# Kernel tuning notes

Hardware: AMD Instinct MI355X
Metric: run time of the kernel (lower is better)

## Reference

```python
import math
import jax, jax.numpy as jnp
import numpy as np

N_HEAD = 16
BLOCK_SIZE = 2048


def setup_inputs() -> dict:
    key = jax.random.key(0)
    ks = jax.random.split(key, 6)
    B, L, D = 2, 2048, 1024
    hs = D // N_HEAD
    s = 0.02
    return {
        "x": jax.random.normal(ks[0], (B, L, D), dtype=jnp.float32),
        "Wqkv": jax.random.normal(ks[1], (D, 3 * D), dtype=jnp.float32) * s,
        "bqkv": jax.random.normal(ks[2], (3 * D,), dtype=jnp.float32) * s,
        "Wproj": jax.random.normal(ks[3], (D, D), dtype=jnp.float32) * s,
        "bproj": jax.random.normal(ks[4], (D,), dtype=jnp.float32) * s,
        "Er": jax.random.normal(ks[5], (BLOCK_SIZE, hs), dtype=jnp.float32),
    }


def _skew(QEr):
    # QEr: [B, H, L, L] -> pad one zero column on the left, reshape, drop first row
    B, H, R, C = QEr.shape
    padded = jnp.pad(QEr, ((0, 0), (0, 0), (0, 0), (1, 0)))  # [B,H,R,C+1]
    reshaped = padded.reshape(B, H, C + 1, R)
    return reshaped[:, :, 1:, :]  # [B,H,R,C]


def reference(x, Wqkv, bqkv, Wproj, bproj, Er):
    B, L, D = x.shape
    H = N_HEAD
    hs = D // H
    qkv = x @ Wqkv + bqkv  # [B,L,3D]
    q, k, v = jnp.split(qkv, 3, axis=-1)
    q = q.reshape(B, L, H, hs).transpose(0, 2, 1, 3)  # [B,H,L,hs]
    k = k.reshape(B, L, H, hs).transpose(0, 2, 1, 3)
    v = v.reshape(B, L, H, hs).transpose(0, 2, 1, 3)

    Er_used = Er[BLOCK_SIZE - L:, :]           # [L, hs]
    QEr = jnp.einsum('bhld,md->bhlm', q, Er_used)  # q @ Er^T -> [B,H,L,L]
    Srel = _skew(QEr)

    scale = 1.0 / math.sqrt(hs)
    att = (jnp.einsum('bhld,bhmd->bhlm', q, k) + Srel) * scale
    causal = jnp.tril(jnp.ones((L, L), dtype=bool))
    att = jnp.where(causal[None, None], att, -jnp.inf)
    att = jax.nn.softmax(att, axis=-1)
    y = jnp.einsum('bhlm,bhmd->bhld', att, v)  # [B,H,L,hs]
    y = y.transpose(0, 2, 1, 3).reshape(B, L, D)
    return y @ Wproj + bproj
```

## Files before the change

kernel.cpp:

```cpp
#include <hip/hip_runtime.h>
#include <hip/hip_bf16.h>

#define LSEQ 2048
#define NH 16
#define HS 64
#define DIM 1024

typedef __attribute__((ext_vector_type(8))) short short8;
typedef __attribute__((ext_vector_type(4))) float f32x4;

typedef const __attribute__((address_space(1))) void g_void_t;
typedef __attribute__((address_space(3))) void s_void_t;

#define QSCALE 0.18033688011112042f

static __device__ __forceinline__ short f2bf(float f) {
  __hip_bfloat16 h = __float2bfloat16(f);
  return __builtin_bit_cast(short, h);
}

static __device__ __forceinline__ float fexp2(float x) {
#if __has_builtin(__builtin_amdgcn_exp2f)
  return __builtin_amdgcn_exp2f(x);
#else
  float r; asm("v_exp_f32 %0, %1" : "=v"(r) : "v"(x)); return r;
#endif
}

template<int CTRL>
static __device__ __forceinline__ float dpp_mov(float x) {
  return __builtin_bit_cast(float,
      __builtin_amdgcn_update_dpp(0, __builtin_bit_cast(int, x), CTRL, 0xF, 0xF, true));
}
static __device__ __forceinline__ float redmax16(float x) {
  x = fmaxf(x, dpp_mov<0xB1>(x));
  x = fmaxf(x, dpp_mov<0x4E>(x));
  x = fmaxf(x, dpp_mov<0x141>(x));
  x = fmaxf(x, dpp_mov<0x140>(x));
  return x;
}
static __device__ __forceinline__ float redsum16(float x) {
  x += dpp_mov<0xB1>(x);
  x += dpp_mov<0x4E>(x);
  x += dpp_mov<0x141>(x);
  x += dpp_mov<0x140>(x);
  return x;
}


__global__ void prep_kernel(const float* __restrict__ x, const float* __restrict__ Er,
                            const float* __restrict__ Wqkv, const float* __restrict__ Wproj,
                            short* __restrict__ xb, short* __restrict__ Erb,
                            short* __restrict__ WqkvT, short* __restrict__ WprojT) {
  __shared__ float tile[64][65];
  int bid = blockIdx.x;
  if (bid < 4224) {
    const float* in; short* out; int i0;
    if (bid < 4096) { in = x;  out = xb;  i0 = bid * 256; }
    else            { in = Er; out = Erb; i0 = (bid - 4096) * 256; }
    int i = i0 + threadIdx.x;
    float4 v = reinterpret_cast<const float4*>(in)[i];
    short4 o;
    o.x = f2bf(v.x); o.y = f2bf(v.y); o.z = f2bf(v.z); o.w = f2bf(v.w);
    reinterpret_cast<short4*>(out)[i] = o;
    return;
  }
  int id = bid - 4224;
  const float* W; short* Wt; int N, tx, ty;
  if (id < 768) { W = Wqkv;  Wt = WqkvT;  N = 3072; tx = id % 48; ty = id / 48; }
  else { id -= 768; W = Wproj; Wt = WprojT; N = 1024; tx = id % 16; ty = id / 16; }
  const int K = 1024;
  int k0 = ty * 64, n0 = tx * 64;
  int t = threadIdx.x;
  int r4 = t >> 6, cc = t & 63;
  for (int i = 0; i < 16; ++i) {
    int row = i * 4 + r4;
    tile[row][cc] = W[(size_t)(k0 + row) * N + (n0 + cc)];
  }
  __syncthreads();
  for (int i = 0; i < 16; ++i) {
    int row = i * 4 + r4;
    Wt[(size_t)(n0 + row) * K + (k0 + cc)] = f2bf(tile[cc][row]);
  }
}


template<int MODE>
__global__ __launch_bounds__(256, 2) void gemm_bt_kernel(
    const short* __restrict__ A, const short* __restrict__ Bt,
    const float* __restrict__ bias, int M, int N, int K,
    short* __restrict__ oq, short* __restrict__ ok, short* __restrict__ ov,
    float* __restrict__ of)
{
  __shared__ short Al[128 * 32];
  __shared__ short Bl[128 * 32];
  const int m0 = blockIdx.y * 128, n0 = blockIdx.x * 128;
  const int t = threadIdx.x;
  const int lane = t & 63, wave = t >> 6;
  const int wr = wave >> 1, wc = wave & 1;
  const int g = lane >> 4, c = lane & 15;
  f32x4 acc[4][4] = {};

  for (int k0 = 0; k0 < K; k0 += 32) {
    __syncthreads();
    for (int i = 0; i < 2; ++i) {
      int ch = i * 256 + t;
      int row = ch >> 2, c8 = ch & 3;
      __builtin_amdgcn_global_load_lds(
          (g_void_t*)(A + (size_t)(m0 + row) * K + k0 + c8 * 8),
          (s_void_t*)(Al + (i * 256 + wave * 64) * 8), 16, 0, 0);
      __builtin_amdgcn_global_load_lds(
          (g_void_t*)(Bt + (size_t)(n0 + row) * K + k0 + c8 * 8),
          (s_void_t*)(Bl + (i * 256 + wave * 64) * 8), 16, 0, 0);
    }
    __syncthreads();
    short8 af[4], bf[4];
#pragma unroll
    for (int mi = 0; mi < 4; ++mi) {
      int row = wr * 64 + mi * 16 + c;
      af[mi] = *reinterpret_cast<const short8*>(Al + row * 32 + g * 8);
    }
#pragma unroll
    for (int ni = 0; ni < 4; ++ni) {
      int row = wc * 64 + ni * 16 + c;
      bf[ni] = *reinterpret_cast<const short8*>(Bl + row * 32 + g * 8);
    }
#pragma unroll
    for (int mi = 0; mi < 4; ++mi)
#pragma unroll
      for (int ni = 0; ni < 4; ++ni)
        acc[mi][ni] = __builtin_amdgcn_mfma_f32_16x16x32_bf16(af[mi], bf[ni], acc[mi][ni], 0, 0, 0);
  }

#pragma unroll
  for (int mi = 0; mi < 4; ++mi)
#pragma unroll
    for (int ni = 0; ni < 4; ++ni) {
      int n = n0 + wc * 64 + ni * 16 + c;
      float bv = bias[n];
#pragma unroll
      for (int r = 0; r < 4; ++r) {
        int m = m0 + wr * 64 + mi * 16 + g * 4 + r;
        float val = acc[mi][ni][r] + bv;
        if (MODE == 0) {
          int which = n >> 10;
          int hh2 = (n >> 6) & 15;
          int d = n & 63;
          int b = m >> 11, ll = m & 2047;
          if (which == 0) {
            oq[(((size_t)b * NH + hh2) * LSEQ + ll) * HS + d] = f2bf(val * QSCALE);
          } else if (which == 1) {
            ok[(((size_t)b * NH + hh2) * LSEQ + ll) * HS + d] = f2bf(val);
          } else {
            ov[(((size_t)b * NH + hh2) * HS + d) * LSEQ + ll] = f2bf(val);
          }
        } else {
          of[(size_t)m * N + n] = val;
        }
      }
    }
}


__global__ __launch_bounds__(256, 2) void attn_kernel(
    const short* __restrict__ Qb, const short* __restrict__ Kb,
    const short* __restrict__ VTb, const short* __restrict__ Erb,
    short* __restrict__ Y)
{
  const int bid = blockIdx.x;
  const int pair = bid >> 5;
  const int bh = bid & 31;
  const int bb = bh >> 4, hh = bh & 15;
  const int t = threadIdx.x;
  const int lane = t & 63, wave = t >> 6;
  const int g = lane >> 4, c = lane & 15;
  const int r8 = lane >> 3;
  const int c16b = (lane & 7) * 16;

  __shared__ short Ql[64 * 64];
  __shared__ short Kl[2][64 * 64];
  __shared__ short Vl[2][64 * 64];
  __shared__ short El[4][64 * 64];
  __shared__ short Pl[4][16 * 64];

  auto process = [&](int qt) {
    const int l0 = qt * 64;
    const int base = 31 - qt;

    const short* Qg = Qb + ((size_t)bh * LSEQ + l0) * HS;
    for (int i = 0; i < 2; ++i) {
      int ch = i * 256 + t;
      int row = ch >> 3, c8 = ch & 7;
      uint4 v = *reinterpret_cast<const uint4*>(Qg + row * HS + c8 * 8);
      int byte = row * 128 + ((c8 * 16) ^ ((row & 7) << 4));
      *reinterpret_cast<uint4*>(reinterpret_cast<char*>(Ql) + byte) = v;
    }
    __syncthreads();

    short8 qf[2];
#pragma unroll
    for (int kk = 0; kk < 2; ++kk) {
      int row = wave * 16 + c;
      int byte = row * 128 + ((kk * 32 + g * 8) * 2 ^ ((row & 7) << 4));
      qf[kk] = *reinterpret_cast<const short8*>(reinterpret_cast<char*>(Ql) + byte);
    }

    f32x4 acc_o[4] = {};
    float mrun[4], lrun[4];
#pragma unroll
    for (int r = 0; r < 4; ++r) { mrun[r] = -1e30f; lrun[r] = 0.0f; }

    auto stage_KV = [&](int step, int sel) {
      const char* Kg = (const char*)(Kb + ((size_t)bh * LSEQ + step * 64) * HS);
#pragma unroll
      for (int j = 0; j < 2; ++j) {
        int row = wave * 16 + j * 8 + r8;
        __builtin_amdgcn_global_load_lds(
            (g_void_t*)(Kg + row * 128 + (c16b ^ ((row & 7) << 4))),
            (s_void_t*)(&Kl[sel][(wave * 16 + j * 8) * 64]), 16, 0, 0);
      }
#pragma unroll
      for (int j = 0; j < 2; ++j) {
        int row = wave * 16 + j * 8 + r8;
        const char* Vg = (const char*)(VTb + ((size_t)bh * HS + row) * LSEQ + step * 64);
        __builtin_amdgcn_global_load_lds(
            (g_void_t*)(Vg + (c16b ^ ((row & 7) << 4))),
            (s_void_t*)(&Vl[sel][(wave * 16 + j * 8) * 64]), 16, 0, 0);
      }
    };
    auto stage_E = [&](int chunk) {
      int slot = chunk & 3;
#pragma unroll
      for (int j = 0; j < 2; ++j) {
        int row = wave * 16 + j * 8 + r8;
        int e = chunk * 64 + row;
        if (e > LSEQ - 1) e = LSEQ - 1;
        __builtin_amdgcn_global_load_lds(
            (g_void_t*)((const char*)Erb + (size_t)e * 128 + (c16b ^ ((row & 7) << 4))),
            (s_void_t*)(&El[slot][(wave * 16 + j * 8) * 64]), 16, 0, 0);
      }
    };

    stage_KV(0, 0);
    stage_E(base);
    stage_E(base + 1);

    for (int s = 0; s <= qt; ++s) {
      const int sel = s & 1;
      const bool diag = (s == qt);

      if (s < qt) {
        stage_KV(s + 1, sel ^ 1);
        stage_E(base + s + 2);
        asm volatile("s_waitcnt vmcnt(6)" ::: "memory");
      } else {
        asm volatile("s_waitcnt vmcnt(0)" ::: "memory");
      }
      __builtin_amdgcn_s_barrier();
      __builtin_amdgcn_sched_barrier(0);

      __builtin_amdgcn_s_setprio(1);
      f32x4 ga[5];
#pragma unroll
      for (int s5 = 0; s5 < 5; ++s5) {
        int rb = ((3 - wave) + s5) * 16 + c;
        int phys = (((base + s + (rb >> 6)) & 3) << 6) | (rb & 63);
        ga[s5] = (f32x4){0.0f, 0.0f, 0.0f, 0.0f};
#pragma unroll
        for (int kk = 0; kk < 2; ++kk) {
          int byte = phys * 128 + (((kk * 32 + g * 8) * 2) ^ ((rb & 7) << 4));
          short8 ef = *reinterpret_cast<const short8*>((char*)El + byte);
          ga[s5] = __builtin_amdgcn_mfma_f32_16x16x32_bf16(qf[kk], ef, ga[s5], 0, 0, 0);
        }
      }

      f32x4 sa[4];
#pragma unroll
      for (int ns = 0; ns < 4; ++ns) {
        sa[ns] = (f32x4){0.0f, 0.0f, 0.0f, 0.0f};
#pragma unroll
        for (int kk = 0; kk < 2; ++kk) {
          int row = ns * 16 + c;
          int byte = row * 128 + (((kk * 32 + g * 8) * 2) ^ ((row & 7) << 4));
          short8 kf = *reinterpret_cast<const short8*>((char*)Kl[sel] + byte);
          sa[ns] = __builtin_amdgcn_mfma_f32_16x16x32_bf16(qf[kk], kf, sa[ns], 0, 0, 0);
        }
      }
      __builtin_amdgcn_s_setprio(0);

      float sv[4][4];
#pragma unroll
      for (int r = 0; r < 4; ++r) {
        int i4 = g * 4 + r;
        int u0 = c + 15 - i4;
        int srcl = (g << 4) | (u0 & 15);
        float bp[5];
#pragma unroll
        for (int s5 = 0; s5 < 5; ++s5) bp[s5] = __shfl(ga[s5][r], srcl, 64);
        bool lo = (u0 < 16);
#pragma unroll
        for (int ns = 0; ns < 4; ++ns) {
          float srel = lo ? bp[ns] : bp[ns + 1];
          float xx = sa[ns][r] + srel;
          if (diag && (ns * 16 + c > wave * 16 + i4)) xx = -1e30f;
          sv[ns][r] = xx;
        }
      }

      float mx[4];
      bool need = false;
#pragma unroll
      for (int r = 0; r < 4; ++r) {
        float m = fmaxf(fmaxf(sv[0][r], sv[1][r]), fmaxf(sv[2][r], sv[3][r]));
        mx[r] = redmax16(m);
        need = need || (mx[r] > mrun[r] + 4.0f);
      }
      if (__ballot(need)) {
#pragma unroll
        for (int r = 0; r < 4; ++r) {
          float mnew = fmaxf(mrun[r], mx[r]);
          float al = fexp2(mrun[r] - mnew);
          mrun[r] = mnew;
          lrun[r] *= al;
#pragma unroll
          for (int ns = 0; ns < 4; ++ns) acc_o[ns][r] *= al;
        }
      }
#pragma unroll
      for (int ns = 0; ns < 4; ++ns)
#pragma unroll
        for (int r = 0; r < 4; ++r)
          sv[ns][r] = fexp2(sv[ns][r] - mrun[r]);
#pragma unroll
      for (int r = 0; r < 4; ++r) {
        float s2 = (sv[0][r] + sv[1][r]) + (sv[2][r] + sv[3][r]);
        lrun[r] += redsum16(s2);
      }

      short* Pw = Pl[wave];
#pragma unroll
      for (int ns = 0; ns < 4; ++ns)
#pragma unroll
        for (int r = 0; r < 4; ++r) {
          int row = g * 4 + r;
          int byte = row * 128 + (((ns * 16 + c) * 2) ^ ((row & 7) << 4));
          *reinterpret_cast<short*>(reinterpret_cast<char*>(Pw) + byte) = f2bf(sv[ns][r]);
        }

      __builtin_amdgcn_s_setprio(1);
#pragma unroll
      for (int kk = 0; kk < 2; ++kk) {
        int kbyte = (kk * 32 + g * 8) * 2;
        int byteP = c * 128 + (kbyte ^ ((c & 7) << 4));
        short8 pf = *reinterpret_cast<const short8*>(reinterpret_cast<char*>(Pw) + byteP);
#pragma unroll
        for (int ns = 0; ns < 4; ++ns) {
          int rowV = ns * 16 + c;
          int byteV = rowV * 128 + (kbyte ^ ((rowV & 7) << 4));
          short8 vf = *reinterpret_cast<const short8*>((char*)Vl[sel] + byteV);
          acc_o[ns] = __builtin_amdgcn_mfma_f32_16x16x32_bf16(pf, vf, acc_o[ns], 0, 0, 0);
        }
      }
      __builtin_amdgcn_s_setprio(0);

      __builtin_amdgcn_sched_barrier(0);
      __builtin_amdgcn_s_barrier();
    }

#pragma unroll
    for (int ns = 0; ns < 4; ++ns)
#pragma unroll
      for (int r = 0; r < 4; ++r) {
        int row = g * 4 + r;
        int lg = l0 + wave * 16 + row;
        int d = ns * 16 + c;
        Y[((size_t)bb * LSEQ + lg) * DIM + hh * HS + d] = f2bf(acc_o[ns][r] / lrun[r]);
      }
  };

  process(31 - pair);
  process(pair);
}


extern "C" void kernel_launch(void* const* d_in, const int* in_sizes, int n_in,
                              void* d_out, int out_size, void* d_ws, size_t ws_size,
                              hipStream_t stream)
{
  const float* x     = (const float*)d_in[0];
  const float* Wqkv  = (const float*)d_in[1];
  const float* bqkv  = (const float*)d_in[2];
  const float* Wproj = (const float*)d_in[3];
  const float* bproj = (const float*)d_in[4];
  const float* Er    = (const float*)d_in[5];

  char* ws = (char*)d_ws;
  short* xb     = (short*)(ws + 0);
  short* WqkvT  = (short*)(ws + 8388608);
  short* WprojT = (short*)(ws + 14680064);
  short* Erb    = (short*)(ws + 16777216);
  short* qB     = (short*)(ws + 17039360);
  short* kB     = (short*)(ws + 25427968);
  short* vTB    = (short*)(ws + 33816576);
  short* yB     = (short*)(ws + 42205184);

  prep_kernel<<<dim3(5248), 256, 0, stream>>>(x, Er, Wqkv, Wproj, xb, Erb, WqkvT, WprojT);

  gemm_bt_kernel<0><<<dim3(3072 / 128, 4096 / 128), 256, 0, stream>>>(
      xb, WqkvT, bqkv, 4096, 3072, 1024, qB, kB, vTB, nullptr);

  attn_kernel<<<dim3(512), 256, 0, stream>>>(qB, kB, vTB, Erb, yB);

  gemm_bt_kernel<1><<<dim3(1024 / 128, 4096 / 128), 256, 0, stream>>>(
      yB, WprojT, bproj, 4096, 1024, 1024, nullptr, nullptr, nullptr, (float*)d_out);
}
```

Measured before the change: 147.7 us.

## Split long causal query tiles across two blocks and merge partial softmax results

The attention kernel stops pairing a long and a short query tile in one block. It launches one block per tile, and the 16 longest tiles per head are split across two blocks that write partial outputs plus running max and sum to workspace. A new merge kernel combines these partials with log-sum-exp rescaling. Separately, the K/V/Er staging drops double buffering in favour of a single buffer loaded after each step, which shrinks LDS so occupancy can rise to 4 blocks. The split adds parallelism and balances load, at the cost of an extra kernel launch, partial-result traffic, bf16 rounding of the partial outputs, and exposed load latency per step.

```diff
diff --git a/kernel.cpp b/kernel.cpp
--- a/kernel.cpp
+++ b/kernel.cpp
@@ -17,6 +17,10 @@
 static __device__ __forceinline__ short f2bf(float f) {
   __hip_bfloat16 h = __float2bfloat16(f);
   return __builtin_bit_cast(short, h);
+}
+static __device__ __forceinline__ float bf2f(short s) {
+  __hip_bfloat16 h = __builtin_bit_cast(__hip_bfloat16, s);
+  return __bfloat162float(h);
 }
 
 static __device__ __forceinline__ float fexp2(float x) {
@@ -162,211 +166,204 @@
 }
 
 
-__global__ __launch_bounds__(256, 2) void attn_kernel(
+#define PART_BYTES 8704
+
+__global__ __launch_bounds__(256, 4) void attn_kernel(
     const short* __restrict__ Qb, const short* __restrict__ Kb,
     const short* __restrict__ VTb, const short* __restrict__ Erb,
-    short* __restrict__ Y)
+    short* __restrict__ Y, char* __restrict__ Part)
 {
   const int bid = blockIdx.x;
-  const int pair = bid >> 5;
+  const int j = bid >> 5;
   const int bh = bid & 31;
   const int bb = bh >> 4, hh = bh & 15;
+
+  int qt, s0, s1, part;
+  bool split;
+  if (j < 32) {
+    qt = 31 - (j >> 1);
+    part = j & 1;
+    int h = (qt + 1) >> 1;
+    s0 = part ? h : 0;
+    s1 = part ? qt + 1 : h;
+    split = true;
+  } else {
+    qt = 47 - j;
+    part = 0; s0 = 0; s1 = qt + 1;
+    split = false;
+  }
+
+  const int l0 = qt * 64;
+  const int base = 31 - qt;
   const int t = threadIdx.x;
   const int lane = t & 63, wave = t >> 6;
   const int g = lane >> 4, c = lane & 15;
   const int r8 = lane >> 3;
   const int c16b = (lane & 7) * 16;
 
-  __shared__ short Ql[64 * 64];
-  __shared__ short Kl[2][64 * 64];
-  __shared__ short Vl[2][64 * 64];
-  __shared__ short El[4][64 * 64];
+  __shared__ short Kl[64 * 64];
+  __shared__ short Vl[64 * 64];
+  __shared__ short El[128 * 64];
   __shared__ short Pl[4][16 * 64];
 
-  auto process = [&](int qt) {
-    const int l0 = qt * 64;
-    const int base = 31 - qt;
-
-    const short* Qg = Qb + ((size_t)bh * LSEQ + l0) * HS;
-    for (int i = 0; i < 2; ++i) {
-      int ch = i * 256 + t;
-      int row = ch >> 3, c8 = ch & 7;
-      uint4 v = *reinterpret_cast<const uint4*>(Qg + row * HS + c8 * 8);
-      int byte = row * 128 + ((c8 * 16) ^ ((row & 7) << 4));
-      *reinterpret_cast<uint4*>(reinterpret_cast<char*>(Ql) + byte) = v;
-    }
-    __syncthreads();
-
-    short8 qf[2];
+  short8 qf[2];
+#pragma unroll
+  for (int kk = 0; kk < 2; ++kk)
+    qf[kk] = *reinterpret_cast<const short8*>(
+        Qb + ((size_t)bh * LSEQ + l0 + wave * 16 + c) * HS + kk * 32 + g * 8);
+
+  auto stage = [&](int step) {
+    const char* Kg = (const char*)(Kb + ((size_t)bh * LSEQ + step * 64) * HS);
+#pragma unroll
+    for (int jj = 0; jj < 2; ++jj) {
+      int row = wave * 16 + jj * 8 + r8;
+      __builtin_amdgcn_global_load_lds(
+          (g_void_t*)(Kg + row * 128 + (c16b ^ ((row & 7) << 4))),
+          (s_void_t*)(&Kl[(wave * 16 + jj * 8) * 64]), 16, 0, 0);
+    }
+#pragma unroll
+    for (int jj = 0; jj < 2; ++jj) {
+      int row = wave * 16 + jj * 8 + r8;
+      const char* Vg = (const char*)(VTb + ((size_t)bh * HS + row) * LSEQ + step * 64);
+      __builtin_amdgcn_global_load_lds(
+          (g_void_t*)(Vg + (c16b ^ ((row & 7) << 4))),
+          (s_void_t*)(&Vl[(wave * 16 + jj * 8) * 64]), 16, 0, 0);
+    }
+#pragma unroll
+    for (int jj = 0; jj < 4; ++jj) {
+      int row = wave * 32 + jj * 8 + r8;
+      int e = (base + step) * 64 + row;
+      if (e > LSEQ - 1) e = LSEQ - 1;
+      __builtin_amdgcn_global_load_lds(
+          (g_void_t*)((const char*)Erb + (size_t)e * 128 + (c16b ^ ((row & 7) << 4))),
+          (s_void_t*)(&El[(wave * 32 + jj * 8) * 64]), 16, 0, 0);
+    }
+  };
+
+  stage(s0);
+
+  f32x4 acc_o[4] = {};
+  float mrun[4], lrun[4];
+#pragma unroll
+  for (int r = 0; r < 4; ++r) { mrun[r] = -1e30f; lrun[r] = 0.0f; }
+
+  for (int s = s0; s < s1; ++s) {
+    const bool diag = (s == qt);
+
+    asm volatile("s_waitcnt vmcnt(0)" ::: "memory");
+    __builtin_amdgcn_s_barrier();
+    __builtin_amdgcn_sched_barrier(0);
+
+    __builtin_amdgcn_s_setprio(1);
+    f32x4 ga[5];
+#pragma unroll
+    for (int s5 = 0; s5 < 5; ++s5) {
+      int rb = ((3 - wave) + s5) * 16 + c;
+      ga[s5] = (f32x4){0.0f, 0.0f, 0.0f, 0.0f};
+#pragma unroll
+      for (int kk = 0; kk < 2; ++kk) {
+        int byte = rb * 128 + (((kk * 32 + g * 8) * 2) ^ ((rb & 7) << 4));
+        short8 ef = *reinterpret_cast<const short8*>((char*)El + byte);
+        ga[s5] = __builtin_amdgcn_mfma_f32_16x16x32_bf16(qf[kk], ef, ga[s5], 0, 0, 0);
+      }
+    }
+
+    f32x4 sa[4];
+#pragma unroll
+    for (int ns = 0; ns < 4; ++ns) {
+      sa[ns] = (f32x4){0.0f, 0.0f, 0.0f, 0.0f};
+#pragma unroll
+      for (int kk = 0; kk < 2; ++kk) {
+        int row = ns * 16 + c;
+        int byte = row * 128 + (((kk * 32 + g * 8) * 2) ^ ((row & 7) << 4));
+        short8 kf = *reinterpret_cast<const short8*>((char*)Kl + byte);
+        sa[ns] = __builtin_amdgcn_mfma_f32_16x16x32_bf16(qf[kk], kf, sa[ns], 0, 0, 0);
+      }
+    }
+    __builtin_amdgcn_s_setprio(0);
+
+    float sv[4][4];
+#pragma unroll
+    for (int r = 0; r < 4; ++r) {
+      int i4 = g * 4 + r;
+      int u0 = c + 15 - i4;
+      int srcl = (g << 4) | (u0 & 15);
+      float bp[5];
+#pragma unroll
+      for (int s5 = 0; s5 < 5; ++s5) bp[s5] = __shfl(ga[s5][r], srcl, 64);
+      bool lo = (u0 < 16);
+#pragma unroll
+      for (int ns = 0; ns < 4; ++ns) {
+        float srel = lo ? bp[ns] : bp[ns + 1];
+        float xx = sa[ns][r] + srel;
+        if (diag && (ns * 16 + c > wave * 16 + i4)) xx = -1e30f;
+        sv[ns][r] = xx;
+      }
+    }
+
+    float mx[4];
+    bool need = false;
+#pragma unroll
+    for (int r = 0; r < 4; ++r) {
+      float m = fmaxf(fmaxf(sv[0][r], sv[1][r]), fmaxf(sv[2][r], sv[3][r]));
+      mx[r] = redmax16(m);
+      need = need || (mx[r] > mrun[r] + 4.0f);
+    }
+    if (__ballot(need)) {
+#pragma unroll
+      for (int r = 0; r < 4; ++r) {
+        float mnew = fmaxf(mrun[r], mx[r]);
+        float al = fexp2(mrun[r] - mnew);
+        mrun[r] = mnew;
+        lrun[r] *= al;
+#pragma unroll
+        for (int ns = 0; ns < 4; ++ns) acc_o[ns][r] *= al;
+      }
+    }
+#pragma unroll
+    for (int ns = 0; ns < 4; ++ns)
+#pragma unroll
+      for (int r = 0; r < 4; ++r)
+        sv[ns][r] = fexp2(sv[ns][r] - mrun[r]);
+#pragma unroll
+    for (int r = 0; r < 4; ++r) {
+      float s2 = (sv[0][r] + sv[1][r]) + (sv[2][r] + sv[3][r]);
+      lrun[r] += redsum16(s2);
+    }
+
+    short* Pw = Pl[wave];
+#pragma unroll
+    for (int ns = 0; ns < 4; ++ns)
+#pragma unroll
+      for (int r = 0; r < 4; ++r) {
+        int row = g * 4 + r;
+        int byte = row * 128 + (((ns * 16 + c) * 2) ^ ((row & 7) << 4));
+        *reinterpret_cast<short*>(reinterpret_cast<char*>(Pw) + byte) = f2bf(sv[ns][r]);
+      }
+
+    __builtin_amdgcn_s_setprio(1);
 #pragma unroll
     for (int kk = 0; kk < 2; ++kk) {
-      int row = wave * 16 + c;
-      int byte = row * 128 + ((kk * 32 + g * 8) * 2 ^ ((row & 7) << 4));
-      qf[kk] = *reinterpret_cast<const short8*>(reinterpret_cast<char*>(Ql) + byte);
-    }
-
-    f32x4 acc_o[4] = {};
-    float mrun[4], lrun[4];
-#pragma unroll
-    for (int r = 0; r < 4; ++r) { mrun[r] = -1e30f; lrun[r] = 0.0f; }
-
-    auto stage_KV = [&](int step, int sel) {
-      const char* Kg = (const char*)(Kb + ((size_t)bh * LSEQ + step * 64) * HS);
-#pragma unroll
-      for (int j = 0; j < 2; ++j) {
-        int row = wave * 16 + j * 8 + r8;
-        __builtin_amdgcn_global_load_lds(
-            (g_void_t*)(Kg + row * 128 + (c16b ^ ((row & 7) << 4))),
-            (s_void_t*)(&Kl[sel][(wave * 16 + j * 8) * 64]), 16, 0, 0);
-      }
-#pragma unroll
-      for (int j = 0; j < 2; ++j) {
-        int row = wave * 16 + j * 8 + r8;
-        const char* Vg = (const char*)(VTb + ((size_t)bh * HS + row) * LSEQ + step * 64);
-        __builtin_amdgcn_global_load_lds(
-            (g_void_t*)(Vg + (c16b ^ ((row & 7) << 4))),
-            (s_void_t*)(&Vl[sel][(wave * 16 + j * 8) * 64]), 16, 0, 0);
-      }
-    };
-    auto stage_E = [&](int chunk) {
-      int slot = chunk & 3;
-#pragma unroll
-      for (int j = 0; j < 2; ++j) {
-        int row = wave * 16 + j * 8 + r8;
-        int e = chunk * 64 + row;
-        if (e > LSEQ - 1) e = LSEQ - 1;
-        __builtin_amdgcn_global_load_lds(
-            (g_void_t*)((const char*)Erb + (size_t)e * 128 + (c16b ^ ((row & 7) << 4))),
-            (s_void_t*)(&El[slot][(wave * 16 + j * 8) * 64]), 16, 0, 0);
-      }
-    };
-
-    stage_KV(0, 0);
-    stage_E(base);
-    stage_E(base + 1);
-
-    for (int s = 0; s <= qt; ++s) {
-      const int sel = s & 1;
-      const bool diag = (s == qt);
-
-      if (s < qt) {
-        stage_KV(s + 1, sel ^ 1);
-        stage_E(base + s + 2);
-        asm volatile("s_waitcnt vmcnt(6)" ::: "memory");
-      } else {
-        asm volatile("s_waitcnt vmcnt(0)" ::: "memory");
-      }
-      __builtin_amdgcn_s_barrier();
-      __builtin_amdgcn_sched_barrier(0);
-
-      __builtin_amdgcn_s_setprio(1);
-      f32x4 ga[5];
-#pragma unroll
-      for (int s5 = 0; s5 < 5; ++s5) {
-        int rb = ((3 - wave) + s5) * 16 + c;
-        int phys = (((base + s + (rb >> 6)) & 3) << 6) | (rb & 63);
-        ga[s5] = (f32x4){0.0f, 0.0f, 0.0f, 0.0f};
-#pragma unroll
-        for (int kk = 0; kk < 2; ++kk) {
-          int byte = phys * 128 + (((kk * 32 + g * 8) * 2) ^ ((rb & 7) << 4));
-          short8 ef = *reinterpret_cast<const short8*>((char*)El + byte);
-          ga[s5] = __builtin_amdgcn_mfma_f32_16x16x32_bf16(qf[kk], ef, ga[s5], 0, 0, 0);
-        }
-      }
-
-      f32x4 sa[4];
+      int kbyte = (kk * 32 + g * 8) * 2;
+      int byteP = c * 128 + (kbyte ^ ((c & 7) << 4));
+      short8 pf = *reinterpret_cast<const short8*>(reinterpret_cast<char*>(Pw) + byteP);
 #pragma unroll
       for (int ns = 0; ns < 4; ++ns) {
-        sa[ns] = (f32x4){0.0f, 0.0f, 0.0f, 0.0f};
-#pragma unroll
-        for (int kk = 0; kk < 2; ++kk) {
-          int row = ns * 16 + c;
-          int byte = row * 128 + (((kk * 32 + g * 8) * 2) ^ ((row & 7) << 4));
-          short8 kf = *reinterpret_cast<const short8*>((char*)Kl[sel] + byte);
-          sa[ns] = __builtin_amdgcn_mfma_f32_16x16x32_bf16(qf[kk], kf, sa[ns], 0, 0, 0);
-        }
-      }
-      __builtin_amdgcn_s_setprio(0);
-
-      float sv[4][4];
-#pragma unroll
-      for (int r = 0; r < 4; ++r) {
-        int i4 = g * 4 + r;
-        int u0 = c + 15 - i4;
-        int srcl = (g << 4) | (u0 & 15);
-        float bp[5];
-#pragma unroll
-        for (int s5 = 0; s5 < 5; ++s5) bp[s5] = __shfl(ga[s5][r], srcl, 64);
-        bool lo = (u0 < 16);
-#pragma unroll
-        for (int ns = 0; ns < 4; ++ns) {
-          float srel = lo ? bp[ns] : bp[ns + 1];
-          float xx = sa[ns][r] + srel;
-          if (diag && (ns * 16 + c > wave * 16 + i4)) xx = -1e30f;
-          sv[ns][r] = xx;
-        }
-      }
-
-      float mx[4];
-      bool need = false;
-#pragma unroll
-      for (int r = 0; r < 4; ++r) {
-        float m = fmaxf(fmaxf(sv[0][r], sv[1][r]), fmaxf(sv[2][r], sv[3][r]));
-        mx[r] = redmax16(m);
-        need = need || (mx[r] > mrun[r] + 4.0f);
-      }
-      if (__ballot(need)) {
-#pragma unroll
-        for (int r = 0; r < 4; ++r) {
-          float mnew = fmaxf(mrun[r], mx[r]);
-          float al = fexp2(mrun[r] - mnew);
-          mrun[r] = mnew;
-          lrun[r] *= al;
-#pragma unroll
-          for (int ns = 0; ns < 4; ++ns) acc_o[ns][r] *= al;
-        }
-      }
-#pragma unroll
-      for (int ns = 0; ns < 4; ++ns)
-#pragma unroll
-        for (int r = 0; r < 4; ++r)
-          sv[ns][r] = fexp2(sv[ns][r] - mrun[r]);
-#pragma unroll
-      for (int r = 0; r < 4; ++r) {
-        float s2 = (sv[0][r] + sv[1][r]) + (sv[2][r] + sv[3][r]);
-        lrun[r] += redsum16(s2);
-      }
-
-      short* Pw = Pl[wave];
-#pragma unroll
-      for (int ns = 0; ns < 4; ++ns)
-#pragma unroll
-        for (int r = 0; r < 4; ++r) {
-          int row = g * 4 + r;
-          int byte = row * 128 + (((ns * 16 + c) * 2) ^ ((row & 7) << 4));
-          *reinterpret_cast<short*>(reinterpret_cast<char*>(Pw) + byte) = f2bf(sv[ns][r]);
-        }
-
-      __builtin_amdgcn_s_setprio(1);
-#pragma unroll
-      for (int kk = 0; kk < 2; ++kk) {
-        int kbyte = (kk * 32 + g * 8) * 2;
-        int byteP = c * 128 + (kbyte ^ ((c & 7) << 4));
-        short8 pf = *reinterpret_cast<const short8*>(reinterpret_cast<char*>(Pw) + byteP);
-#pragma unroll
-        for (int ns = 0; ns < 4; ++ns) {
-          int rowV = ns * 16 + c;
-          int byteV = rowV * 128 + (kbyte ^ ((rowV & 7) << 4));
-          short8 vf = *reinterpret_cast<const short8*>((char*)Vl[sel] + byteV);
-          acc_o[ns] = __builtin_amdgcn_mfma_f32_16x16x32_bf16(pf, vf, acc_o[ns], 0, 0, 0);
-        }
-      }
-      __builtin_amdgcn_s_setprio(0);
-
-      __builtin_amdgcn_sched_barrier(0);
-      __builtin_amdgcn_s_barrier();
-    }
-
+        int rowV = ns * 16 + c;
+        int byteV = rowV * 128 + (kbyte ^ ((rowV & 7) << 4));
+        short8 vf = *reinterpret_cast<const short8*>((char*)Vl + byteV);
+        acc_o[ns] = __builtin_amdgcn_mfma_f32_16x16x32_bf16(pf, vf, acc_o[ns], 0, 0, 0);
+      }
+    }
+    __builtin_amdgcn_s_setprio(0);
+
+    __builtin_amdgcn_sched_barrier(0);
+    __builtin_amdgcn_s_barrier();
+
+    if (s + 1 < s1) stage(s + 1);
+  }
+
+  if (!split) {
 #pragma unroll
     for (int ns = 0; ns < 4; ++ns)
 #pragma unroll
@@ -376,10 +373,59 @@
         int d = ns * 16 + c;
         Y[((size_t)bb * LSEQ + lg) * DIM + hh * HS + d] = f2bf(acc_o[ns][r] / lrun[r]);
       }
-  };
-
-  process(31 - pair);
-  process(pair);
+  } else {
+    int sp = (qt - 16) * 32 + bh;
+    char* pb = Part + (size_t)(sp * 2 + part) * PART_BYTES;
+    short* Op = (short*)pb;
+    float* mp = (float*)(pb + 8192);
+    float* lp = (float*)(pb + 8448);
+#pragma unroll
+    for (int r = 0; r < 4; ++r) {
+      int row = wave * 16 + g * 4 + r;
+#pragma unroll
+      for (int ns = 0; ns < 4; ++ns)
+        Op[row * 64 + ns * 16 + c] = f2bf(acc_o[ns][r]);
+      if (c == 0) { mp[row] = mrun[r]; lp[row] = lrun[r]; }
+    }
+  }
+}
+
+
+__global__ void merge_kernel(const char* __restrict__ Part, short* __restrict__ Y) {
+  int sp = blockIdx.x;
+  int qt = 16 + (sp >> 5);
+  int bh = sp & 31;
+  int bb = bh >> 4, hh = bh & 15;
+  int t = threadIdx.x;
+  int row = t >> 2, cg = t & 3;
+
+  const char* p0 = Part + (size_t)(sp * 2) * PART_BYTES;
+  const char* p1 = p0 + PART_BYTES;
+  float m0 = *(const float*)(p0 + 8192 + row * 4);
+  float l0 = *(const float*)(p0 + 8448 + row * 4);
+  float m1 = *(const float*)(p1 + 8192 + row * 4);
+  float l1 = *(const float*)(p1 + 8448 + row * 4);
+  float M = fmaxf(m0, m1);
+  float a0 = fexp2(m0 - M), a1 = fexp2(m1 - M);
+  float inv = 1.0f / (l0 * a0 + l1 * a1);
+
+  const short* O0 = (const short*)p0 + row * 64 + cg * 16;
+  const short* O1 = (const short*)p1 + row * 64 + cg * 16;
+  short out[16];
+#pragma unroll
+  for (int v = 0; v < 2; ++v) {
+    short8 s0v = *reinterpret_cast<const short8*>(O0 + v * 8);
+    short8 s1v = *reinterpret_cast<const short8*>(O1 + v * 8);
+#pragma unroll
+    for (int e = 0; e < 8; ++e) {
+      float y = (bf2f(s0v[e]) * a0 + bf2f(s1v[e]) * a1) * inv;
+      out[v * 8 + e] = f2bf(y);
+    }
+  }
+  int lg = qt * 64 + row;
+  short* dst = Y + ((size_t)bb * LSEQ + lg) * DIM + hh * HS + cg * 16;
+  *reinterpret_cast<short8*>(dst) = *reinterpret_cast<short8*>(out);
+  *reinterpret_cast<short8*>(dst + 8) = *reinterpret_cast<short8*>(out + 8);
 }
 
 
@@ -403,13 +449,16 @@
   short* kB     = (short*)(ws + 25427968);
   short* vTB    = (short*)(ws + 33816576);
   short* yB     = (short*)(ws + 42205184);
+  char*  Part   = ws;
 
   prep_kernel<<<dim3(5248), 256, 0, stream>>>(x, Er, Wqkv, Wproj, xb, Erb, WqkvT, WprojT);
 
   gemm_bt_kernel<0><<<dim3(3072 / 128, 4096 / 128), 256, 0, stream>>>(
       xb, WqkvT, bqkv, 4096, 3072, 1024, qB, kB, vTB, nullptr);
 
-  attn_kernel<<<dim3(512), 256, 0, stream>>>(qB, kB, vTB, Erb, yB);
+  attn_kernel<<<dim3(1536), 256, 0, stream>>>(qB, kB, vTB, Erb, yB, Part);
+
+  merge_kernel<<<dim3(512), 256, 0, stream>>>(Part, yB);
 
   gemm_bt_kernel<1><<<dim3(1024 / 128, 4096 / 128), 256, 0, stream>>>(
       yB, WprojT, bproj, 4096, 1024, 1024, nullptr, nullptr, nullptr, (float*)d_out);
```

Result: slower. 222.3 us (+50.5%).
